# Kernel optimization log

Hardware: AMD Instinct MI355X
Metric: run time of the kernel (lower is better)

## Reference

```python
import jax, jax.numpy as jnp
import numpy as np

J, E = 17, 4096
LN_EPS = 1e-5

BONE_PAIRS = np.array([[0,1],[1,2],[2,3],[0,4],[4,5],[5,6],[0,7],[7,8],[8,9],[9,10],
                       [8,11],[11,12],[12,13],[8,14],[14,15],[15,16]], dtype=np.int32)

def _xavier(key, fan_in, fan_out, gain=0.5):
    limit = gain * np.sqrt(6.0 / (fan_in + fan_out))
    return jax.random.uniform(key, (fan_in, fan_out), jnp.float32, -limit, limit)

def setup_inputs() -> dict:
    key = jax.random.key(0)
    k0, k1, k2 = jax.random.split(key, 3)
    return {
        "joint_embeddings": jax.random.normal(k0, (J, E), jnp.float32) * 0.02,
        "W1": _xavier(k1, 2 * E, E),
        "b1": jnp.zeros((E,), jnp.float32),
        "g1": jnp.ones((E,), jnp.float32),
        "be1": jnp.zeros((E,), jnp.float32),
        "W2": _xavier(k2, E, E),
        "b2": jnp.zeros((E,), jnp.float32),
        "g2": jnp.ones((E,), jnp.float32),
        "be2": jnp.zeros((E,), jnp.float32),
        "bone_pairs": jnp.asarray(BONE_PAIRS),
    }

def _layernorm(x, g, b):
    mu = jnp.mean(x, axis=-1, keepdims=True)
    var = jnp.mean(jnp.square(x - mu), axis=-1, keepdims=True)
    return (x - mu) * jax.lax.rsqrt(var + LN_EPS) * g + b

def reference(joint_embeddings, W1, b1, g1, be1, W2, b2, g2, be2, bone_pairs):
    # L2-normalize each joint embedding (torch F.normalize, eps=1e-12), scale by sqrt(E)
    norm = jnp.linalg.norm(joint_embeddings, axis=-1, keepdims=True)
    joint_emb = joint_embeddings / jnp.maximum(norm, 1e-12)
    joint_emb = joint_emb * jnp.sqrt(jnp.float32(E))
    # gather both endpoints of each bone, concat -> [16, 2E]
    pair_emb = jnp.concatenate([joint_emb[bone_pairs[:, 0]], joint_emb[bone_pairs[:, 1]]], axis=-1)
    # 2-layer MLP with LayerNorm; Dropout(0.1) is identity in eval
    h = jax.nn.relu(_layernorm(pair_emb @ W1 + b1, g1, be1))
    bone_features = _layernorm(h @ W2 + b2, g2, be2)
    return (joint_emb, bone_features)
```

## Files before the change

### kernel.cpp

```cpp
#include <hip/hip_runtime.h>
#include <math.h>

#define J 17
#define E 4096
#define M 16
#define LN_EPS 1e-5f

__global__ void norm17_kernel(const float* __restrict__ je, float* __restrict__ out) {
    const int row = blockIdx.x;
    const float* __restrict__ src = je + (size_t)row * E;
    float* __restrict__ dst = out + (size_t)row * E;

    float ss = 0.0f;
    float4 v[4];
    #pragma unroll
    for (int i = 0; i < 4; ++i) {
        int idx = threadIdx.x + i * 256;
        v[i] = ((const float4*)src)[idx];
        ss += v[i].x * v[i].x + v[i].y * v[i].y + v[i].z * v[i].z + v[i].w * v[i].w;
    }
    for (int off = 32; off; off >>= 1) ss += __shfl_down(ss, off, 64);
    __shared__ float red[4];
    if ((threadIdx.x & 63) == 0) red[threadIdx.x >> 6] = ss;
    __syncthreads();
    float total = red[0] + red[1] + red[2] + red[3];

    float scale = 64.0f / fmaxf(sqrtf(total), 1e-12f);
    #pragma unroll
    for (int i = 0; i < 4; ++i) {
        int idx = threadIdx.x + i * 256;
        float4 o = v[i];
        o.x *= scale; o.y *= scale; o.z *= scale; o.w *= scale;
        ((float4*)dst)[idx] = o;
    }
}

#define DO_GROUP(KB, W0, W1, W2, W3)                                  \
    {                                                                 \
        _Pragma("unroll")                                             \
        for (int m = 0; m < M; ++m) {                                 \
            const float4 xv = *(const float4*)&xs[m][(KB)];           \
            acc[m].x = fmaf(xv.x, W0.x, acc[m].x);                    \
            acc[m].x = fmaf(xv.y, W1.x, acc[m].x);                    \
            acc[m].x = fmaf(xv.z, W2.x, acc[m].x);                    \
            acc[m].x = fmaf(xv.w, W3.x, acc[m].x);                    \
            acc[m].y = fmaf(xv.x, W0.y, acc[m].y);                    \
            acc[m].y = fmaf(xv.y, W1.y, acc[m].y);                    \
            acc[m].y = fmaf(xv.z, W2.y, acc[m].y);                    \
            acc[m].y = fmaf(xv.w, W3.y, acc[m].y);                    \
        }                                                             \
    }

template <int KTOT, int KC, bool GATHER, bool PARTIAL>
__global__ __launch_bounds__(256) void gemm_kernel(
        const float* __restrict__ X,
        const float* __restrict__ W,
        float* __restrict__ part,
        const int* __restrict__ pairs,
        const float* __restrict__ joint) {

    __shared__ float xs[M][KC];
    const int k0 = blockIdx.y * KC;

    for (int s = threadIdx.x; s < M * KC / 4; s += 256) {
        const int m  = s / (KC / 4);
        const int k4 = s % (KC / 4);
        const float* srow;
        if (GATHER) {
            const int half = (k0 >= E) ? 1 : 0;
            srow = joint + (size_t)pairs[2 * m + half] * E + (k0 & (E - 1));
        } else {
            srow = X + (size_t)m * KTOT + k0;
        }
        ((float4*)&xs[m][0])[k4] = ((const float4*)srow)[k4];
    }
    __syncthreads();

    const int col = blockIdx.x * 512 + (threadIdx.x << 1);
    const float* __restrict__ wp = W + (size_t)k0 * E + col;

    float2 acc[M];
    #pragma unroll
    for (int m = 0; m < M; ++m) acc[m] = make_float2(0.f, 0.f);

    float2 wa0 = *(const float2*)(wp + (size_t)0 * E);
    float2 wa1 = *(const float2*)(wp + (size_t)1 * E);
    float2 wa2 = *(const float2*)(wp + (size_t)2 * E);
    float2 wa3 = *(const float2*)(wp + (size_t)3 * E);
    float2 wb0 = *(const float2*)(wp + (size_t)4 * E);
    float2 wb1 = *(const float2*)(wp + (size_t)5 * E);
    float2 wb2 = *(const float2*)(wp + (size_t)6 * E);
    float2 wb3 = *(const float2*)(wp + (size_t)7 * E);

    int kk = 0;
    for (; kk + 8 < KC; kk += 8) {
        DO_GROUP(kk, wa0, wa1, wa2, wa3);
        wa0 = *(const float2*)(wp + (size_t)(kk + 8)  * E);
        wa1 = *(const float2*)(wp + (size_t)(kk + 9)  * E);
        wa2 = *(const float2*)(wp + (size_t)(kk + 10) * E);
        wa3 = *(const float2*)(wp + (size_t)(kk + 11) * E);
        DO_GROUP(kk + 4, wb0, wb1, wb2, wb3);
        wb0 = *(const float2*)(wp + (size_t)(kk + 12) * E);
        wb1 = *(const float2*)(wp + (size_t)(kk + 13) * E);
        wb2 = *(const float2*)(wp + (size_t)(kk + 14) * E);
        wb3 = *(const float2*)(wp + (size_t)(kk + 15) * E);
    }
    DO_GROUP(kk,     wa0, wa1, wa2, wa3);
    DO_GROUP(kk + 4, wb0, wb1, wb2, wb3);

    if (PARTIAL) {
        float* dst = part + ((size_t)blockIdx.y * M) * E + col;
        #pragma unroll
        for (int m = 0; m < M; ++m) {
            *(float2*)(dst + (size_t)m * E) = acc[m];
        }
    } else {
        #pragma unroll
        for (int m = 0; m < M; ++m) {
            atomicAdd(&part[(size_t)m * E + col + 0], acc[m].x);
            atomicAdd(&part[(size_t)m * E + col + 1], acc[m].y);
        }
    }
}

template <int CHUNKS>
__global__ __launch_bounds__(64) void reduce_kernel(const float* __restrict__ part,
                                                    float* __restrict__ pre) {
    const size_t f = ((size_t)blockIdx.x * 64 + threadIdx.x) * 4;
    const float* p = part + f;
    float4 s0 = make_float4(0.f, 0.f, 0.f, 0.f);
    float4 s1 = s0, s2 = s0, s3 = s0;
    #pragma unroll 8
    for (int c = 0; c < CHUNKS; c += 4) {
        const float4 a = *(const float4*)(p + (size_t)(c + 0) * (M * E));
        const float4 b = *(const float4*)(p + (size_t)(c + 1) * (M * E));
        const float4 d = *(const float4*)(p + (size_t)(c + 2) * (M * E));
        const float4 e = *(const float4*)(p + (size_t)(c + 3) * (M * E));
        s0.x += a.x; s0.y += a.y; s0.z += a.z; s0.w += a.w;
        s1.x += b.x; s1.y += b.y; s1.z += b.z; s1.w += b.w;
        s2.x += d.x; s2.y += d.y; s2.z += d.z; s2.w += d.w;
        s3.x += e.x; s3.y += e.y; s3.z += e.z; s3.w += e.w;
    }
    float4 o;
    o.x = (s0.x + s1.x) + (s2.x + s3.x);
    o.y = (s0.y + s1.y) + (s2.y + s3.y);
    o.z = (s0.z + s1.z) + (s2.z + s3.z);
    o.w = (s0.w + s1.w) + (s2.w + s3.w);
    *(float4*)(pre + f) = o;
}

__global__ void ln_row_kernel(const float* __restrict__ pre,
                              const float* __restrict__ bias,
                              const float* __restrict__ g,
                              const float* __restrict__ be,
                              float* __restrict__ out,
                              int relu) {
    const int r = blockIdx.x;
    const float* __restrict__ src = pre + (size_t)r * E;

    float4 v[4];
    float s = 0.0f, s2 = 0.0f;
    #pragma unroll
    for (int i = 0; i < 4; ++i) {
        int idx = threadIdx.x + i * 256;
        float4 p = ((const float4*)src)[idx];
        float4 b = ((const float4*)bias)[idx];
        p.x += b.x; p.y += b.y; p.z += b.z; p.w += b.w;
        v[i] = p;
        s  += p.x + p.y + p.z + p.w;
        s2 += p.x * p.x + p.y * p.y + p.z * p.z + p.w * p.w;
    }
    for (int off = 32; off; off >>= 1) {
        s  += __shfl_down(s,  off, 64);
        s2 += __shfl_down(s2, off, 64);
    }
    __shared__ float ra[4], rb[4];
    if ((threadIdx.x & 63) == 0) { ra[threadIdx.x >> 6] = s; rb[threadIdx.x >> 6] = s2; }
    __syncthreads();
    s  = ra[0] + ra[1] + ra[2] + ra[3];
    s2 = rb[0] + rb[1] + rb[2] + rb[3];

    const float mu  = s * (1.0f / E);
    const float var = s2 * (1.0f / E) - mu * mu;
    const float rs  = rsqrtf(var + LN_EPS);

    #pragma unroll
    for (int i = 0; i < 4; ++i) {
        int idx = threadIdx.x + i * 256;
        float4 gg = ((const float4*)g)[idx];
        float4 bb = ((const float4*)be)[idx];
        float4 o;
        o.x = (v[i].x - mu) * rs * gg.x + bb.x;
        o.y = (v[i].y - mu) * rs * gg.y + bb.y;
        o.z = (v[i].z - mu) * rs * gg.z + bb.z;
        o.w = (v[i].w - mu) * rs * gg.w + bb.w;
        if (relu) {
            o.x = fmaxf(o.x, 0.0f); o.y = fmaxf(o.y, 0.0f);
            o.z = fmaxf(o.z, 0.0f); o.w = fmaxf(o.w, 0.0f);
        }
        ((float4*)(out + (size_t)r * E))[idx] = o;
    }
}

extern "C" void kernel_launch(void* const* d_in, const int* in_sizes, int n_in,
                              void* d_out, int out_size, void* d_ws, size_t ws_size,
                              hipStream_t stream) {
    const float* je  = (const float*)d_in[0];
    const float* W1  = (const float*)d_in[1];
    const float* b1  = (const float*)d_in[2];
    const float* g1  = (const float*)d_in[3];
    const float* be1 = (const float*)d_in[4];
    const float* W2  = (const float*)d_in[5];
    const float* b2  = (const float*)d_in[6];
    const float* g2  = (const float*)d_in[7];
    const float* be2 = (const float*)d_in[8];
    const int*   bp  = (const int*)d_in[9];

    float* out       = (float*)d_out;
    float* joint_out = out;
    float* bone_out  = out + J * E;

    const size_t part_floats = (size_t)128 * M * E;
    const size_t need = (part_floats + 3 * (size_t)M * E) * sizeof(float);

    norm17_kernel<<<J, 256, 0, stream>>>(je, joint_out);

    if (ws_size >= need) {
        float* part = (float*)d_ws;
        float* pre1 = part + part_floats;
        float* pre2 = pre1 + (size_t)M * E;
        float* h    = pre2 + (size_t)M * E;

        gemm_kernel<2 * E, 64, true, true><<<dim3(8, 128), 256, 0, stream>>>(
            nullptr, W1, part, bp, joint_out);
        reduce_kernel<128><<<256, 64, 0, stream>>>(part, pre1);
        ln_row_kernel<<<M, 256, 0, stream>>>(pre1, b1, g1, be1, h, 1);

        gemm_kernel<E, 32, false, true><<<dim3(8, 128), 256, 0, stream>>>(
            h, W2, part, nullptr, nullptr);
        reduce_kernel<128><<<256, 64, 0, stream>>>(part, pre2);
        ln_row_kernel<<<M, 256, 0, stream>>>(pre2, b2, g2, be2, bone_out, 0);
    } else {
        float* pre1 = (float*)d_ws;
        float* pre2 = pre1 + (size_t)M * E;
        float* h    = pre2 + (size_t)M * E;
        hipMemsetAsync(d_ws, 0, 2 * (size_t)M * E * sizeof(float), stream);

        gemm_kernel<2 * E, 64, true, false><<<dim3(8, 128), 256, 0, stream>>>(
            nullptr, W1, pre1, bp, joint_out);
        ln_row_kernel<<<M, 256, 0, stream>>>(pre1, b1, g1, be1, h, 1);
        gemm_kernel<E, 32, false, false><<<dim3(8, 128), 256, 0, stream>>>(
            h, W2, pre2, nullptr, nullptr);
        ln_row_kernel<<<M, 256, 0, stream>>>(pre2, b2, g2, be2, bone_out, 0);
    }
}
```

Before: 297.1 us.

## Widen GEMM columns per thread and fuse first LayerNorm into reduce and GEMM2

Each GEMM thread now computes 8 output columns instead of 2, using float4 weight loads, so the grid shrinks from 8x128 to 2x128 blocks. The first LayerNorm kernel is removed: the reduce kernel adds the bias and accumulates per-row sum and sum-of-squares with atomics, and the second GEMM applies normalize+ReLU while staging its input. This cuts one launch and one pass over the hidden activations. In exchange it holds more accumulator registers, gives less parallelism for a memory-bound weight stream, and computes variance as E[x^2]-mu^2, which is less numerically robust.

```diff
diff --git a/kernel.cpp b/kernel.cpp
--- a/kernel.cpp
+++ b/kernel.cpp
@@ -35,29 +35,40 @@
     }
 }
 
-#define DO_GROUP(KB, W0, W1, W2, W3)                                  \
+#define DO2(KB, WL0, WH0, WL1, WH1)                                   \
     {                                                                 \
         _Pragma("unroll")                                             \
         for (int m = 0; m < M; ++m) {                                 \
-            const float4 xv = *(const float4*)&xs[m][(KB)];           \
-            acc[m].x = fmaf(xv.x, W0.x, acc[m].x);                    \
-            acc[m].x = fmaf(xv.y, W1.x, acc[m].x);                    \
-            acc[m].x = fmaf(xv.z, W2.x, acc[m].x);                    \
-            acc[m].x = fmaf(xv.w, W3.x, acc[m].x);                    \
-            acc[m].y = fmaf(xv.x, W0.y, acc[m].y);                    \
-            acc[m].y = fmaf(xv.y, W1.y, acc[m].y);                    \
-            acc[m].y = fmaf(xv.z, W2.y, acc[m].y);                    \
-            acc[m].y = fmaf(xv.w, W3.y, acc[m].y);                    \
+            const float2 xv = *(const float2*)&xs[m][(KB)];           \
+            accL[m].x = fmaf(xv.x, WL0.x, accL[m].x);                 \
+            accL[m].y = fmaf(xv.x, WL0.y, accL[m].y);                 \
+            accL[m].z = fmaf(xv.x, WL0.z, accL[m].z);                 \
+            accL[m].w = fmaf(xv.x, WL0.w, accL[m].w);                 \
+            accH[m].x = fmaf(xv.x, WH0.x, accH[m].x);                 \
+            accH[m].y = fmaf(xv.x, WH0.y, accH[m].y);                 \
+            accH[m].z = fmaf(xv.x, WH0.z, accH[m].z);                 \
+            accH[m].w = fmaf(xv.x, WH0.w, accH[m].w);                 \
+            accL[m].x = fmaf(xv.y, WL1.x, accL[m].x);                 \
+            accL[m].y = fmaf(xv.y, WL1.y, accL[m].y);                 \
+            accL[m].z = fmaf(xv.y, WL1.z, accL[m].z);                 \
+            accL[m].w = fmaf(xv.y, WL1.w, accL[m].w);                 \
+            accH[m].x = fmaf(xv.y, WH1.x, accH[m].x);                 \
+            accH[m].y = fmaf(xv.y, WH1.y, accH[m].y);                 \
+            accH[m].z = fmaf(xv.y, WH1.z, accH[m].z);                 \
+            accH[m].w = fmaf(xv.y, WH1.w, accH[m].w);                 \
         }                                                             \
     }
 
-template <int KTOT, int KC, bool GATHER, bool PARTIAL>
+template <int KTOT, int KC, bool GATHER, bool PARTIAL, bool LNSTAGE>
 __global__ __launch_bounds__(256) void gemm_kernel(
         const float* __restrict__ X,
         const float* __restrict__ W,
         float* __restrict__ part,
         const int* __restrict__ pairs,
-        const float* __restrict__ joint) {
+        const float* __restrict__ joint,
+        const float* __restrict__ lng,
+        const float* __restrict__ lnb,
+        const float* __restrict__ stats) {
 
     __shared__ float xs[M][KC];
     const int k0 = blockIdx.y * KC;
@@ -65,67 +76,92 @@
     for (int s = threadIdx.x; s < M * KC / 4; s += 256) {
         const int m  = s / (KC / 4);
         const int k4 = s % (KC / 4);
-        const float* srow;
         if (GATHER) {
             const int half = (k0 >= E) ? 1 : 0;
-            srow = joint + (size_t)pairs[2 * m + half] * E + (k0 & (E - 1));
+            const float* srow = joint + (size_t)pairs[2 * m + half] * E + (k0 & (E - 1));
+            ((float4*)&xs[m][0])[k4] = ((const float4*)srow)[k4];
+        } else if (LNSTAGE) {
+            const float4 v  = ((const float4*)(X + (size_t)m * KTOT + k0))[k4];
+            const float4 gg = ((const float4*)(lng + k0))[k4];
+            const float4 bb = ((const float4*)(lnb + k0))[k4];
+            const float mu  = stats[2 * m] * (1.0f / E);
+            const float var = stats[2 * m + 1] * (1.0f / E) - mu * mu;
+            const float rs  = rsqrtf(var + LN_EPS);
+            float4 h;
+            h.x = fmaxf((v.x - mu) * rs * gg.x + bb.x, 0.0f);
+            h.y = fmaxf((v.y - mu) * rs * gg.y + bb.y, 0.0f);
+            h.z = fmaxf((v.z - mu) * rs * gg.z + bb.z, 0.0f);
+            h.w = fmaxf((v.w - mu) * rs * gg.w + bb.w, 0.0f);
+            ((float4*)&xs[m][0])[k4] = h;
         } else {
-            srow = X + (size_t)m * KTOT + k0;
-        }
-        ((float4*)&xs[m][0])[k4] = ((const float4*)srow)[k4];
+            const float* srow = X + (size_t)m * KTOT + k0;
+            ((float4*)&xs[m][0])[k4] = ((const float4*)srow)[k4];
+        }
     }
     __syncthreads();
 
-    const int col = blockIdx.x * 512 + (threadIdx.x << 1);
+    const int col = blockIdx.x * 2048 + (threadIdx.x << 3);
     const float* __restrict__ wp = W + (size_t)k0 * E + col;
 
-    float2 acc[M];
-    #pragma unroll
-    for (int m = 0; m < M; ++m) acc[m] = make_float2(0.f, 0.f);
-
-    float2 wa0 = *(const float2*)(wp + (size_t)0 * E);
-    float2 wa1 = *(const float2*)(wp + (size_t)1 * E);
-    float2 wa2 = *(const float2*)(wp + (size_t)2 * E);
-    float2 wa3 = *(const float2*)(wp + (size_t)3 * E);
-    float2 wb0 = *(const float2*)(wp + (size_t)4 * E);
-    float2 wb1 = *(const float2*)(wp + (size_t)5 * E);
-    float2 wb2 = *(const float2*)(wp + (size_t)6 * E);
-    float2 wb3 = *(const float2*)(wp + (size_t)7 * E);
+    float4 accL[M], accH[M];
+    #pragma unroll
+    for (int m = 0; m < M; ++m) {
+        accL[m] = make_float4(0.f, 0.f, 0.f, 0.f);
+        accH[m] = make_float4(0.f, 0.f, 0.f, 0.f);
+    }
+
+    float4 aL0 = *(const float4*)(wp + (size_t)0 * E);
+    float4 aH0 = *(const float4*)(wp + (size_t)0 * E + 4);
+    float4 aL1 = *(const float4*)(wp + (size_t)1 * E);
+    float4 aH1 = *(const float4*)(wp + (size_t)1 * E + 4);
+    float4 bL0 = *(const float4*)(wp + (size_t)2 * E);
+    float4 bH0 = *(const float4*)(wp + (size_t)2 * E + 4);
+    float4 bL1 = *(const float4*)(wp + (size_t)3 * E);
+    float4 bH1 = *(const float4*)(wp + (size_t)3 * E + 4);
 
     int kk = 0;
-    for (; kk + 8 < KC; kk += 8) {
-        DO_GROUP(kk, wa0, wa1, wa2, wa3);
-        wa0 = *(const float2*)(wp + (size_t)(kk + 8)  * E);
-        wa1 = *(const float2*)(wp + (size_t)(kk + 9)  * E);
-        wa2 = *(const float2*)(wp + (size_t)(kk + 10) * E);
-        wa3 = *(const float2*)(wp + (size_t)(kk + 11) * E);
-        DO_GROUP(kk + 4, wb0, wb1, wb2, wb3);
-        wb0 = *(const float2*)(wp + (size_t)(kk + 12) * E);
-        wb1 = *(const float2*)(wp + (size_t)(kk + 13) * E);
-        wb2 = *(const float2*)(wp + (size_t)(kk + 14) * E);
-        wb3 = *(const float2*)(wp + (size_t)(kk + 15) * E);
-    }
-    DO_GROUP(kk,     wa0, wa1, wa2, wa3);
-    DO_GROUP(kk + 4, wb0, wb1, wb2, wb3);
+    for (; kk + 4 < KC; kk += 4) {
+        DO2(kk, aL0, aH0, aL1, aH1);
+        aL0 = *(const float4*)(wp + (size_t)(kk + 4) * E);
+        aH0 = *(const float4*)(wp + (size_t)(kk + 4) * E + 4);
+        aL1 = *(const float4*)(wp + (size_t)(kk + 5) * E);
+        aH1 = *(const float4*)(wp + (size_t)(kk + 5) * E + 4);
+        DO2(kk + 2, bL0, bH0, bL1, bH1);
+        bL0 = *(const float4*)(wp + (size_t)(kk + 6) * E);
+        bH0 = *(const float4*)(wp + (size_t)(kk + 6) * E + 4);
+        bL1 = *(const float4*)(wp + (size_t)(kk + 7) * E);
+        bH1 = *(const float4*)(wp + (size_t)(kk + 7) * E + 4);
+    }
+    DO2(kk,     aL0, aH0, aL1, aH1);
+    DO2(kk + 2, bL0, bH0, bL1, bH1);
 
     if (PARTIAL) {
         float* dst = part + ((size_t)blockIdx.y * M) * E + col;
         #pragma unroll
         for (int m = 0; m < M; ++m) {
-            *(float2*)(dst + (size_t)m * E) = acc[m];
+            *(float4*)(dst + (size_t)m * E)     = accL[m];
+            *(float4*)(dst + (size_t)m * E + 4) = accH[m];
         }
     } else {
         #pragma unroll
         for (int m = 0; m < M; ++m) {
-            atomicAdd(&part[(size_t)m * E + col + 0], acc[m].x);
-            atomicAdd(&part[(size_t)m * E + col + 1], acc[m].y);
-        }
-    }
-}
-
-template <int CHUNKS>
+            atomicAdd(&part[(size_t)m * E + col + 0], accL[m].x);
+            atomicAdd(&part[(size_t)m * E + col + 1], accL[m].y);
+            atomicAdd(&part[(size_t)m * E + col + 2], accL[m].z);
+            atomicAdd(&part[(size_t)m * E + col + 3], accL[m].w);
+            atomicAdd(&part[(size_t)m * E + col + 4], accH[m].x);
+            atomicAdd(&part[(size_t)m * E + col + 5], accH[m].y);
+            atomicAdd(&part[(size_t)m * E + col + 6], accH[m].z);
+            atomicAdd(&part[(size_t)m * E + col + 7], accH[m].w);
+        }
+    }
+}
+
+template <int CHUNKS, bool STATS>
 __global__ __launch_bounds__(64) void reduce_kernel(const float* __restrict__ part,
-                                                    float* __restrict__ pre) {
+                                                    float* __restrict__ pre,
+                                                    const float* __restrict__ bias,
+                                                    float* __restrict__ stats) {
     const size_t f = ((size_t)blockIdx.x * 64 + threadIdx.x) * 4;
     const float* p = part + f;
     float4 s0 = make_float4(0.f, 0.f, 0.f, 0.f);
@@ -146,7 +182,25 @@
     o.y = (s0.y + s1.y) + (s2.y + s3.y);
     o.z = (s0.z + s1.z) + (s2.z + s3.z);
     o.w = (s0.w + s1.w) + (s2.w + s3.w);
-    *(float4*)(pre + f) = o;
+
+    if (STATS) {
+        const float4 b = *(const float4*)(bias + (f & (E - 1)));
+        o.x += b.x; o.y += b.y; o.z += b.z; o.w += b.w;
+        *(float4*)(pre + f) = o;
+        float s  = o.x + o.y + o.z + o.w;
+        float sq = o.x * o.x + o.y * o.y + o.z * o.z + o.w * o.w;
+        for (int off = 32; off; off >>= 1) {
+            s  += __shfl_down(s,  off, 64);
+            sq += __shfl_down(sq, off, 64);
+        }
+        if (threadIdx.x == 0) {
+            const int m = (int)(f >> 12);
+            atomicAdd(&stats[2 * m],     s);
+            atomicAdd(&stats[2 * m + 1], sq);
+        }
+    } else {
+        *(float4*)(pre + f) = o;
+    }
 }
 
 __global__ void ln_row_kernel(const float* __restrict__ pre,
@@ -221,24 +275,25 @@
     float* bone_out  = out + J * E;
 
     const size_t part_floats = (size_t)128 * M * E;
-    const size_t need = (part_floats + 3 * (size_t)M * E) * sizeof(float);
+    const size_t need = (part_floats + 2 * (size_t)M * E + 32) * sizeof(float);
 
     norm17_kernel<<<J, 256, 0, stream>>>(je, joint_out);
 
     if (ws_size >= need) {
-        float* part = (float*)d_ws;
-        float* pre1 = part + part_floats;
-        float* pre2 = pre1 + (size_t)M * E;
-        float* h    = pre2 + (size_t)M * E;
-
-        gemm_kernel<2 * E, 64, true, true><<<dim3(8, 128), 256, 0, stream>>>(
-            nullptr, W1, part, bp, joint_out);
-        reduce_kernel<128><<<256, 64, 0, stream>>>(part, pre1);
-        ln_row_kernel<<<M, 256, 0, stream>>>(pre1, b1, g1, be1, h, 1);
-
-        gemm_kernel<E, 32, false, true><<<dim3(8, 128), 256, 0, stream>>>(
-            h, W2, part, nullptr, nullptr);
-        reduce_kernel<128><<<256, 64, 0, stream>>>(part, pre2);
+        float* part  = (float*)d_ws;
+        float* pre1  = part + part_floats;
+        float* pre2  = pre1 + (size_t)M * E;
+        float* stats = pre2 + (size_t)M * E;
+
+        hipMemsetAsync(stats, 0, 32 * sizeof(float), stream);
+
+        gemm_kernel<2 * E, 64, true, true, false><<<dim3(2, 128), 256, 0, stream>>>(
+            nullptr, W1, part, bp, joint_out, nullptr, nullptr, nullptr);
+        reduce_kernel<128, true><<<256, 64, 0, stream>>>(part, pre1, b1, stats);
+
+        gemm_kernel<E, 32, false, true, true><<<dim3(2, 128), 256, 0, stream>>>(
+            pre1, W2, part, nullptr, nullptr, g1, be1, stats);
+        reduce_kernel<128, false><<<256, 64, 0, stream>>>(part, pre2, nullptr, nullptr);
         ln_row_kernel<<<M, 256, 0, stream>>>(pre2, b2, g2, be2, bone_out, 0);
     } else {
         float* pre1 = (float*)d_ws;
@@ -246,11 +301,11 @@
         float* h    = pre2 + (size_t)M * E;
         hipMemsetAsync(d_ws, 0, 2 * (size_t)M * E * sizeof(float), stream);
 
-        gemm_kernel<2 * E, 64, true, false><<<dim3(8, 128), 256, 0, stream>>>(
-            nullptr, W1, pre1, bp, joint_out);
+        gemm_kernel<2 * E, 64, true, false, false><<<dim3(2, 128), 256, 0, stream>>>(
+            nullptr, W1, pre1, bp, joint_out, nullptr, nullptr, nullptr);
         ln_row_kernel<<<M, 256, 0, stream>>>(pre1, b1, g1, be1, h, 1);
-        gemm_kernel<E, 32, false, false><<<dim3(8, 128), 256, 0, stream>>>(
-            h, W2, pre2, nullptr, nullptr);
+        gemm_kernel<E, 32, false, false, false><<<dim3(2, 128), 256, 0, stream>>>(
+            h, W2, pre2, nullptr, nullptr, nullptr, nullptr, nullptr);
         ln_row_kernel<<<M, 256, 0, stream>>>(pre2, b2, g2, be2, bone_out, 0);
     }
 }
```

New measurement: 296.7 us. Within noise of the previous version (-0.1%).
